# Kernel optimization log

Measured on AMD Instinct MI355X. Metric: run time of the kernel, lower is better.

Reference implementation:

```python
import jax, jax.numpy as jnp
import numpy as np

NUM_LAYERS = 3
N = 4096
DIM = 512
TOPK = 8
BIG = 1.0e9
EPS_COS = 1e-8
EPS_NORM = 1e-12
BN_EPS = 1e-5
LAM_K = 64.0
LAM_Z = 16.0
SIGMA_INTRA = 0.99
ALPHA = np.linspace(1.0, 1.2, NUM_LAYERS)
BETA = np.linspace(0.0, 0.0, NUM_LAYERS)


def setup_inputs() -> dict:
    key = jax.random.key(0)
    ks = jax.random.split(key, 6)
    feats = jax.random.normal(ks[0], (NUM_LAYERS, N, DIM), dtype=jnp.float32)
    labels = jax.random.randint(ks[1], (N,), 0, 64, dtype=jnp.int64)
    fc1_w = jax.random.normal(ks[2], (NUM_LAYERS, DIM, DIM), dtype=jnp.float32) * (1.0 / np.sqrt(DIM))
    fc2_w = jax.random.normal(ks[3], (NUM_LAYERS, DIM, DIM), dtype=jnp.float32) * (1.0 / np.sqrt(DIM))
    bn_gamma = jnp.ones((NUM_LAYERS, DIM), dtype=jnp.float32)
    bn_beta = jnp.zeros((NUM_LAYERS, DIM), dtype=jnp.float32)
    proj_w = jax.random.normal(ks[4], (768, DIM), dtype=jnp.float32) * (1.0 / np.sqrt(DIM))
    return {"feats": feats, "labels": labels, "fc1_w": fc1_w, "fc2_w": fc2_w,
            "bn_gamma": bn_gamma, "bn_beta": bn_beta, "proj_w": proj_w}


def _l2norm(x, axis=-1):
    return x / jnp.maximum(jnp.linalg.norm(x, axis=axis, keepdims=True), EPS_NORM)


def _pairwise_cosine(G):
    Gn = _l2norm(G)
    sim = Gn @ Gn.T
    return jnp.clip(sim, -1.0 + EPS_COS, 1.0 - EPS_COS)


def _knn_mask(sim, base_mask, topk):
    n = sim.shape[0]
    masked = (sim - BIG * jnp.eye(n, dtype=sim.dtype)) * base_mask - (1.0 - base_mask) * BIG
    k = min(topk, max(n - 1, 1))
    idx = jax.lax.top_k(masked, k)[1]  # [N, k]
    st = jnp.zeros_like(sim).at[jnp.arange(n)[:, None], idx].set(1.0)
    return jnp.maximum(st, st.T)


def _build_intra_inter(sim, labels, topk):
    same = (labels[None, :] == labels[:, None]).astype(sim.dtype)
    diff = 1.0 - same
    m_intra = _knn_mask(sim, same, topk)
    m_inter = _knn_mask(sim, diff, topk)
    sim_intra = jnp.maximum(sim * m_intra, 0.0)
    sim_inter = jnp.maximum(sim * m_inter, 0.0)
    return sim_intra, sim_inter


def _normalize_sym(sim_graph, eps=1e-8):
    d = jnp.maximum(sim_graph.sum(axis=1), eps)
    dinv = d ** -0.5
    return dinv[:, None] * sim_graph * dinv[None, :]  # == diag(dinv) @ S @ diag(dinv)


def _diffusion(K, t_diff=1):
    out = K
    for _ in range(max(t_diff - 1, 0)):
        out = out @ K
    return out


def _bn_train(x, gamma, beta):
    m = x.mean(axis=0)
    v = x.var(axis=0)  # biased, as torch BN training
    return (x - m) / jnp.sqrt(v + BN_EPS) * gamma + beta


def _gam(S, G, w1, w2, gamma, beta):
    Z = S @ (G @ w1.T)
    Z = jax.nn.relu(_bn_train(Z, gamma, beta))
    Z = S @ (Z @ w2.T)
    return Z + G


def reference(feats, labels, fc1_w, fc2_w, bn_gamma, bn_beta, proj_w):
    n = feats.shape[1]
    eye = jnp.eye(n, dtype=feats.dtype)
    same = (labels[None, :] == labels[:, None]).astype(feats.dtype)

    K_list, Z_list = [], []
    for i in range(NUM_LAYERS):
        G = feats[i]
        sim = _pairwise_cosine(G)
        sim_intra, sim_inter = _build_intra_inter(sim, labels, TOPK)
        sim_graph = float(ALPHA[i]) * sim_intra + float(BETA[i]) * sim_inter + 1e-6 * eye
        S = _normalize_sym(sim_graph)
        K = _diffusion(S, t_diff=1)
        Z = _gam(S, G, fc1_w[i], fc2_w[i], bn_gamma[i], bn_beta[i])
        K_list.append(K)
        Z_list.append(Z)

    loss_K = jnp.zeros((), dtype=feats.dtype)
    loss_Z = jnp.zeros((), dtype=feats.dtype)
    for i in range(1, NUM_LAYERS):
        K_tgt = jax.lax.stop_gradient(K_list[i])
        loss_K = loss_K + jnp.mean((K_list[i - 1] - K_tgt) ** 2)
        Zp = _l2norm(Z_list[i - 1] @ proj_w.T)
        Zc = _l2norm(Z_list[i] @ proj_w.T)
        loss_Z = loss_Z + jnp.mean((Zp - jax.lax.stop_gradient(Zc)) ** 2)

    K_idea = _diffusion(same * SIGMA_INTRA, t_diff=1)
    loss_idea = jnp.mean((K_list[-1] - K_idea) ** 2)
    return LAM_K * loss_K + LAM_Z * loss_Z + loss_idea
```

## Files before the change

kernel.cpp:

```cpp
#include <hip/hip_runtime.h>
#include <math.h>
#include <stdint.h>

#define NROWS 4096
#define DIM   512
#define NCLS  64
#define CAP   128
#define PD    768
#define NL    3
#define PARTSZ (size_t)(NCLS * 4 * 1024)

typedef __attribute__((ext_vector_type(8))) short short8v;
typedef __attribute__((ext_vector_type(4))) float f32x4;

__device__ __forceinline__ unsigned short f2bf(float f) {
  unsigned u = __float_as_uint(f);
  unsigned r = (u + 0x7FFF + ((u >> 16) & 1)) >> 16;
  return (unsigned short)r;
}

__device__ __forceinline__ void gload_lds16(const void* g, void* l) {
  auto* lp = reinterpret_cast<__attribute__((address_space(3))) unsigned int*>(
      reinterpret_cast<uintptr_t>(l));
  const auto* gp = reinterpret_cast<const __attribute__((address_space(1))) unsigned int*>(
      reinterpret_cast<uintptr_t>(g));
  __builtin_amdgcn_global_load_lds(gp, lp, 16, 0, 0);
}

__device__ __forceinline__ float waveReduce(float v) {
#pragma unroll
  for (int o = 32; o > 0; o >>= 1) v += __shfl_down(v, o);
  return v;
}

__device__ __forceinline__ float blockReduce(float v) {
  __shared__ float sh[4];
  int lane = threadIdx.x & 63, wv = threadIdx.x >> 6;
  v = waveReduce(v);
  if (lane == 0) sh[wv] = v;
  __syncthreads();
  float t = 0.f;
  if (threadIdx.x == 0) {
    int nw = (blockDim.x + 63) >> 6;
    for (int i = 0; i < nw; ++i) t += sh[i];
  }
  return t;
}

__global__ __launch_bounds__(256) void k_hist(const int* __restrict__ labels, int* __restrict__ chunkCnt) {
  __shared__ int h[NCLS];
  int t = threadIdx.x;
  if (t < NCLS) h[t] = 0;
  __syncthreads();
  atomicAdd(&h[labels[blockIdx.x * 256 + t]], 1);
  __syncthreads();
  if (t < NCLS) chunkCnt[blockIdx.x * NCLS + t] = h[t];
}

__global__ void k_scan(const int* __restrict__ chunkCnt, int* __restrict__ cnt,
                       int* __restrict__ off, int* __restrict__ chunkBase, float* __restrict__ acc) {
  __shared__ int sc[NCLS];
  int c = threadIdx.x;
  if (c < 8) acc[c] = 0.f;
  int tot = 0;
  for (int b = 0; b < 16; ++b) tot += chunkCnt[b * NCLS + c];
  cnt[c] = tot;
  sc[c] = tot;
  __syncthreads();
  if (c == 0) {
    int s = 0;
    for (int i = 0; i < NCLS; ++i) { int tv = sc[i]; sc[i] = s; s += tv; }
  }
  __syncthreads();
  int run = sc[c];
  off[c] = run;
  for (int b = 0; b < 16; ++b) { chunkBase[b * NCLS + c] = run; run += chunkCnt[b * NCLS + c]; }
  if (c == 0) off[NCLS] = NROWS;
}

__global__ __launch_bounds__(256) void k_scatter(const int* __restrict__ labels, const int* __restrict__ chunkBase,
                                                 int* __restrict__ perm, int* __restrict__ clsp) {
  __shared__ int lab[256];
  int t = threadIdx.x;
  int r = blockIdx.x * 256 + t;
  int c = labels[r];
  lab[t] = c;
  __syncthreads();
  int rank = 0;
  for (int j = 0; j < t; ++j) rank += (lab[j] == c);
  int pos = chunkBase[blockIdx.x * NCLS + c] + rank;
  perm[pos] = r;
  clsp[pos] = c;
}

__global__ __launch_bounds__(128) void k_prepw(const float* __restrict__ feats, const int* __restrict__ perm,
                                               unsigned short* __restrict__ Gpb, float* __restrict__ invn,
                                               const float4* __restrict__ fc1, const float4* __restrict__ fc2,
                                               const float4* __restrict__ proj,
                                               ushort4* __restrict__ w1, ushort4* __restrict__ w2,
                                               ushort4* __restrict__ pj, float* __restrict__ rnorm) {
  int y = blockIdx.y;
  if (y == NL) {
    const int nW = NL * DIM * DIM / 4;
    const int nP = PD * DIM / 4;
    int idx = blockIdx.x * 128 + threadIdx.x;
    const float4* src; ushort4* dst; int k;
    if (idx < nW) { src = fc1; dst = w1; k = idx; }
    else if (idx < 2 * nW) { src = fc2; dst = w2; k = idx - nW; }
    else if (idx < 2 * nW + nP) { src = proj; dst = pj; k = idx - 2 * nW; }
    else {
      int z = idx - (2 * nW + nP);
      if (z < NL * NROWS) rnorm[z] = 0.f;
      return;
    }
    float4 v = src[k];
    ushort4 o;
    o.x = f2bf(v.x); o.y = f2bf(v.y); o.z = f2bf(v.z); o.w = f2bf(v.w);
    dst[k] = o;
    return;
  }
  __shared__ float red[2];
  int l = y;
  const float* G = feats + (size_t)l * NROWS * DIM;
  unsigned short* Gp = Gpb + (size_t)l * NROWS * DIM;
  int row = blockIdx.x, t = threadIdx.x;
  const float4* src = (const float4*)(G + (size_t)perm[row] * DIM);
  float4 v = src[t];
  ushort4 b;
  b.x = f2bf(v.x); b.y = f2bf(v.y); b.z = f2bf(v.z); b.w = f2bf(v.w);
  *(ushort4*)(Gp + (size_t)row * DIM + t * 4) = b;
  float ss = v.x * v.x + v.y * v.y + v.z * v.z + v.w * v.w;
  ss = waveReduce(ss);
  if ((t & 63) == 0) red[t >> 6] = ss;
  __syncthreads();
  if (t == 0) invn[l * NROWS + row] = 1.f / fmaxf(sqrtf(red[0] + red[1]), 1e-12f);
}

__global__ __launch_bounds__(256) void k_sim(const unsigned short* __restrict__ Gpb,
                                             const float* __restrict__ invn,
                                             const int* __restrict__ cnt, const int* __restrict__ off,
                                             float* __restrict__ sim) {
  int l = blockIdx.z;
  const unsigned short* Gp = Gpb + (size_t)l * NROWS * DIM;
  const float* inv = invn + (size_t)l * NROWS;
  float* sm = sim + (size_t)l * NCLS * CAP * CAP;
  int c = blockIdx.y;
  int n = min(cnt[c], CAP);
  int ti = blockIdx.x >> 2, tj = blockIdx.x & 3;
  if (ti * 32 >= n || tj * 32 >= n) return;
  int base = off[c];
  __shared__ short As[32][40];
  __shared__ short Bs[32][40];
  const int t = threadIdx.x;
  const int lane = t & 63, wv = t >> 6;
  const int qi = wv >> 1, qj = wv & 1;
  const int fr = lane & 15, kg = lane >> 4;
  const int half = t >> 7, tt = t & 127;
  const int srow = tt >> 2, scol = (tt & 3) * 8;
  int gr = (half ? tj : ti) * 32 + srow;
  const unsigned short* ps = Gp + (size_t)(base + min(gr, n - 1)) * DIM + scol;
  short* dst = half ? &Bs[srow][scol] : &As[srow][scol];
  f32x4 acc = {};
  for (int k0 = 0; k0 < DIM; k0 += 32) {
    short8v v = *(const short8v*)(ps + k0);
    __syncthreads();
    *(short8v*)dst = v;
    __syncthreads();
    short8v af = *(const short8v*)&As[qi * 16 + fr][kg * 8];
    short8v bf = *(const short8v*)&Bs[qj * 16 + fr][kg * 8];
    acc = __builtin_amdgcn_mfma_f32_16x16x32_bf16(af, bf, acc, 0, 0, 0);
  }
  int gj = tj * 32 + qj * 16 + fr;
  int r0 = ti * 32 + qi * 16 + kg * 4;
  if (gj < n) {
    float sj = inv[base + gj];
#pragma unroll
    for (int r = 0; r < 4; ++r) {
      int gi = r0 + r;
      if (gi < n) {
        float v = acc[r] * inv[base + gi] * sj;
        v = fminf(fmaxf(v, -1.0f + 1e-8f), 1.0f - 1e-8f);
        sm[((size_t)c * CAP + gi) * CAP + gj] = v;
      }
    }
  }
}

__global__ __launch_bounds__(256) void k_topk(const float* __restrict__ sim, const int* __restrict__ cnt,
                                              const int* __restrict__ off, const int* __restrict__ clsp,
                                              int* __restrict__ t8) {
  int l = blockIdx.y;
  const float* sm = sim + (size_t)l * NCLS * CAP * CAP;
  int* t8l = t8 + (size_t)l * NROWS * 8;
  int pr = blockIdx.x * 256 + threadIdx.x;
  if (pr >= NROWS) return;
  int c = clsp[pr];
  int n = min(cnt[c], CAP);
  int loc = pr - off[c];
  const float4* row4 = (const float4*)(sm + ((size_t)c * CAP + loc) * CAP);
  float bv[8]; int bi[8];
#pragma unroll
  for (int q = 0; q < 8; ++q) { bv[q] = -3e38f; bi[q] = -1; }
  for (int j4 = 0; j4 < CAP / 4; ++j4) {
    if (j4 * 4 >= n) break;
    float4 v4 = row4[j4];
    float vv[4] = {v4.x, v4.y, v4.z, v4.w};
#pragma unroll
    for (int k = 0; k < 4; ++k) {
      int j = j4 * 4 + k;
      if (j >= n || j == loc) continue;
      float v = vv[k];
      if (v > bv[7]) {
        bv[7] = v; bi[7] = j;
#pragma unroll
        for (int q = 7; q > 0; --q) {
          if (bv[q] > bv[q - 1]) {
            float tv = bv[q]; bv[q] = bv[q - 1]; bv[q - 1] = tv;
            int tq = bi[q]; bi[q] = bi[q - 1]; bi[q - 1] = tq;
          }
        }
      }
    }
  }
#pragma unroll
  for (int q = 0; q < 8; ++q) t8l[pr * 8 + q] = bi[q];
}

__global__ __launch_bounds__(256) void k_buildS1(const float* __restrict__ sim, const int* __restrict__ cnt,
                                                 const int* __restrict__ off, const int* __restrict__ t8,
                                                 float* __restrict__ S, float* __restrict__ dinv) {
  int l = blockIdx.z;
  float alpha = 1.0f + 0.1f * l;
  const float* sm = sim + (size_t)l * NCLS * CAP * CAP;
  float* Sl = S + (size_t)l * NCLS * CAP * CAP;
  const int* t8l = t8 + (size_t)l * NROWS * 8;
  float* dv = dinv + (size_t)l * NCLS * CAP;
  int c = blockIdx.x;
  int n = min(cnt[c], CAP);
  int i0 = blockIdx.y * 32;
  if (i0 >= n) return;
  int base = off[c];
  __shared__ int sh8[CAP * 8];
  for (int i = threadIdx.x; i < n * 8; i += 256) sh8[i] = t8l[base * 8 + i];
  __syncthreads();
  int r = threadIdx.x >> 3;
  int lj = threadIdx.x & 7;
  int i = i0 + r;
  float d = 0.f;
  if (i < n) {
    int my8[8];
#pragma unroll
    for (int q = 0; q < 8; ++q) my8[q] = sh8[i * 8 + q];
    const float* srow = sm + ((size_t)c * CAP + i) * CAP;
    float* wrow = Sl + ((size_t)c * CAP + i) * CAP;
    for (int j = lj; j < n; j += 8) {
      float w;
      if (j == i) w = 1e-6f;
      else {
        bool m = false;
#pragma unroll
        for (int q = 0; q < 8; ++q) m = m || (my8[q] == j) || (sh8[j * 8 + q] == i);
        w = m ? alpha * fmaxf(srow[j], 0.f) : 0.f;
      }
      wrow[j] = w;
      d += w;
    }
  }
  d += __shfl_xor(d, 1);
  d += __shfl_xor(d, 2);
  d += __shfl_xor(d, 4);
  if (lj == 0 && i < n) dv[c * CAP + i] = 1.f / sqrtf(fmaxf(d, 1e-8f));
}

__global__ __launch_bounds__(256) void k_buildS2(float* __restrict__ S, const float* __restrict__ dinv,
                                                 const int* __restrict__ cnt) {
  int l = blockIdx.z;
  float* Sl = S + (size_t)l * NCLS * CAP * CAP;
  const float* dv = dinv + (size_t)l * NCLS * CAP;
  int c = blockIdx.x;
  int n = min(cnt[c], CAP);
  int i0 = blockIdx.y * 32;
  if (i0 >= n) return;
  __shared__ float sd[CAP];
  for (int k = threadIdx.x; k < n; k += 256) sd[k] = dv[c * CAP + k];
  __syncthreads();
  for (int p = threadIdx.x; p < 32 * CAP; p += 256) {
    int r = p >> 7, j = p & (CAP - 1);
    int i = i0 + r;
    if (i < n && j < n)
      Sl[((size_t)c * CAP + i) * CAP + j] *= sd[i] * sd[j];
  }
}

__global__ __launch_bounds__(256) void k_gemm_bf16(const short* __restrict__ A, const short* __restrict__ B,
                                                   float* __restrict__ C, float* __restrict__ rnorm, int N,
                                                   long sA, long sB, long sC) {
  int l = blockIdx.z;
  A += (size_t)l * sA; B += (size_t)l * sB; C += (size_t)l * sC;
  if (rnorm) rnorm += (size_t)l * NROWS;
  __shared__ __align__(16) short As[128][32];
  __shared__ __align__(16) short Bs[64][32];
  const int row0 = blockIdx.x * 128, col0 = blockIdx.y * 64;
  const int t = threadIdx.x;
  const int lane = t & 63, wv = t >> 6;
  const int fr = lane & 15, kg = lane >> 4;
  const int srow = lane >> 2, skb = (lane & 3) * 8;
  const short* pa = A + (size_t)(row0 + wv * 32 + srow) * DIM + skb;
  const short* pb = B + (size_t)(col0 + wv * 16 + srow) * DIM + skb;
  f32x4 acc[2][4] = {};
  for (int kt = 0; kt < DIM; kt += 32) {
    __syncthreads();
    gload_lds16(pa + kt, &As[wv * 32][0]);
    gload_lds16(pa + kt + (size_t)16 * DIM, &As[wv * 32 + 16][0]);
    gload_lds16(pb + kt, &Bs[wv * 16][0]);
    __syncthreads();
    short8v af[2], bf[4];
#pragma unroll
    for (int i = 0; i < 2; ++i) af[i] = *(const short8v*)&As[wv * 32 + i * 16 + fr][kg * 8];
#pragma unroll
    for (int j = 0; j < 4; ++j) bf[j] = *(const short8v*)&Bs[j * 16 + fr][kg * 8];
#pragma unroll
    for (int i = 0; i < 2; ++i)
#pragma unroll
      for (int j = 0; j < 4; ++j)
        acc[i][j] = __builtin_amdgcn_mfma_f32_16x16x32_bf16(af[i], bf[j], acc[i][j], 0, 0, 0);
  }
#pragma unroll
  for (int i = 0; i < 2; ++i) {
    int r0 = row0 + wv * 32 + i * 16 + kg * 4;
#pragma unroll
    for (int j = 0; j < 4; ++j) {
      int cc = col0 + j * 16 + fr;
#pragma unroll
      for (int r = 0; r < 4; ++r)
        C[(size_t)(r0 + r) * N + cc] = acc[i][j][r];
    }
    if (rnorm) {
#pragma unroll
      for (int r = 0; r < 4; ++r) {
        float ss = acc[i][0][r] * acc[i][0][r] + acc[i][1][r] * acc[i][1][r] +
                   acc[i][2][r] * acc[i][2][r] + acc[i][3][r] * acc[i][3][r];
        ss += __shfl_xor(ss, 1);
        ss += __shfl_xor(ss, 2);
        ss += __shfl_xor(ss, 4);
        ss += __shfl_xor(ss, 8);
        if (fr == 0) atomicAdd(&rnorm[r0 + r], ss);
      }
    }
  }
}

__global__ __launch_bounds__(256) void k_spmm32p(const float* __restrict__ S, const float* __restrict__ X,
                                                 const float* __restrict__ Gfeat, const int* __restrict__ perm,
                                                 float* __restrict__ Y, unsigned short* __restrict__ Yb,
                                                 float* __restrict__ part,
                                                 const int* __restrict__ cnt, const int* __restrict__ off) {
  int l = blockIdx.z >> 2;
  int zc = blockIdx.z & 3;
  const float* Sl = S + (size_t)l * NCLS * CAP * CAP;
  const float4* X4 = (const float4*)(X + (size_t)l * NROWS * DIM);
  const float4* G4 = Gfeat ? (const float4*)(Gfeat + (size_t)l * NROWS * DIM) : (const float4*)nullptr;
  float4* Y4 = Y ? (float4*)(Y + (size_t)l * NROWS * DIM) : (float4*)nullptr;
  ushort4* Yb4 = Yb ? (ushort4*)(Yb + (size_t)l * NROWS * DIM) : (ushort4*)nullptr;
  int c = blockIdx.x;
  int n = min(cnt[c], CAP);
  int i0 = zc * 32;
  float* pslot = part ? part + (size_t)l * PARTSZ + (size_t)(c * 4 + zc) * 1024 : (float*)nullptr;
  __shared__ float sS[32][CAP];
  if (i0 >= n) {
    if (pslot) {
      int col = blockIdx.y * 256 + threadIdx.x;
      pslot[col] = 0.f;
      pslot[512 + col] = 0.f;
    }
    return;
  }
  int base = off[c];
  int lane = threadIdx.x & 63;
  int col4 = blockIdx.y * 64 + lane;
  int ty = threadIdx.x >> 6;
  {
    const float4* S4 = (const float4*)(Sl + ((size_t)c * CAP + i0) * CAP);
    float4* sS4 = (float4*)&sS[0][0];
    for (int idx = threadIdx.x; idx < 32 * (CAP / 4); idx += 256) {
      int r = idx >> 5;
      sS4[idx] = (i0 + r < n) ? S4[idx] : make_float4(0.f, 0.f, 0.f, 0.f);
    }
  }
  __syncthreads();
  float4 acc[8];
#pragma unroll
  for (int ii = 0; ii < 8; ++ii) acc[ii] = make_float4(0.f, 0.f, 0.f, 0.f);
  size_t xbase = (size_t)base * 128 + col4;
  int n4 = n & ~3;
  float4 x0, x1, x2, x3;
  if (n4 > 0) {
    x0 = X4[xbase];
    x1 = X4[xbase + 128];
    x2 = X4[xbase + 256];
    x3 = X4[xbase + 384];
  }
  for (int j = 0; j < n4; j += 4) {
    float4 nx0, nx1, nx2, nx3;
    int jn = j + 4;
    if (jn < n4) {
      size_t b2 = xbase + (size_t)jn * 128;
      nx0 = X4[b2];
      nx1 = X4[b2 + 128];
      nx2 = X4[b2 + 256];
      nx3 = X4[b2 + 384];
    }
#pragma unroll
    for (int ii = 0; ii < 8; ++ii) {
      float4 s4 = *(const float4*)&sS[ty * 8 + ii][j];
      acc[ii].x += s4.x * x0.x; acc[ii].y += s4.x * x0.y; acc[ii].z += s4.x * x0.z; acc[ii].w += s4.x * x0.w;
      acc[ii].x += s4.y * x1.x; acc[ii].y += s4.y * x1.y; acc[ii].z += s4.y * x1.z; acc[ii].w += s4.y * x1.w;
      acc[ii].x += s4.z * x2.x; acc[ii].y += s4.z * x2.y; acc[ii].z += s4.z * x2.z; acc[ii].w += s4.z * x2.w;
      acc[ii].x += s4.w * x3.x; acc[ii].y += s4.w * x3.y; acc[ii].z += s4.w * x3.z; acc[ii].w += s4.w * x3.w;
    }
    x0 = nx0; x1 = nx1; x2 = nx2; x3 = nx3;
  }
  for (int j = n4; j < n; ++j) {
    float4 x = X4[xbase + (size_t)j * 128];
#pragma unroll
    for (int ii = 0; ii < 8; ++ii) {
      float s = sS[ty * 8 + ii][j];
      acc[ii].x += s * x.x;
      acc[ii].y += s * x.y;
      acc[ii].z += s * x.z;
      acc[ii].w += s * x.w;
    }
  }
  float s1[4] = {0.f, 0.f, 0.f, 0.f}, s2[4] = {0.f, 0.f, 0.f, 0.f};
#pragma unroll
  for (int ii = 0; ii < 8; ++ii) {
    int r = i0 + ty * 8 + ii;
    if (r < n) {
      size_t o = (size_t)(base + r) * 128 + col4;
      float4 v = acc[ii];
      if (G4) {
        float4 g = G4[(size_t)perm[base + r] * 128 + col4];
        v.x += g.x; v.y += g.y; v.z += g.z; v.w += g.w;
      }
      if (pslot) {
        s1[0] += v.x; s1[1] += v.y; s1[2] += v.z; s1[3] += v.w;
        s2[0] += v.x * v.x; s2[1] += v.y * v.y; s2[2] += v.z * v.z; s2[3] += v.w * v.w;
      }
      if (Yb4) {
        ushort4 ob;
        ob.x = f2bf(v.x); ob.y = f2bf(v.y); ob.z = f2bf(v.z); ob.w = f2bf(v.w);
        Yb4[o] = ob;
      } else {
        Y4[o] = v;
      }
    }
  }
  if (pslot) {
    __syncthreads();
    float* scr = &sS[0][0];
#pragma unroll
    for (int q = 0; q < 4; ++q) {
      scr[(ty * 64 + lane) * 8 + q] = s1[q];
      scr[(ty * 64 + lane) * 8 + 4 + q] = s2[q];
    }
    __syncthreads();
    if (ty == 0) {
#pragma unroll
      for (int q = 0; q < 4; ++q) {
        float a = 0.f, b = 0.f;
#pragma unroll
        for (int g = 0; g < 4; ++g) {
          a += scr[(g * 64 + lane) * 8 + q];
          b += scr[(g * 64 + lane) * 8 + 4 + q];
        }
        int col = blockIdx.y * 256 + lane * 4 + q;
        pslot[col] = a;
        pslot[512 + col] = b;
      }
    }
  }
}

__global__ __launch_bounds__(64) void k_bnfin(const float* __restrict__ part, const float* __restrict__ gamma,
                                              const float* __restrict__ beta, float* __restrict__ sc) {
  int l = blockIdx.y;
  const float* pl = part + (size_t)l * PARTSZ;
  int k = blockIdx.x * 64 + threadIdx.x;
  float s = 0.f, s2 = 0.f;
  for (int b = 0; b < NCLS * 4; ++b) {
    s += pl[b * 1024 + k];
    s2 += pl[b * 1024 + 512 + k];
  }
  float m = s * (1.f / NROWS);
  float var = s2 * (1.f / NROWS) - m * m;
  float sg = gamma[l * DIM + k] / sqrtf(var + 1e-5f);
  sc[l * 2 * DIM + k] = sg;
  sc[l * 2 * DIM + DIM + k] = beta[l * DIM + k] - m * sg;
}

__global__ __launch_bounds__(256) void k_bnrelu(const float4* __restrict__ X, const float* __restrict__ sc,
                                                ushort4* __restrict__ Yb) {
  int l = blockIdx.y;
  const float4* Xl = X + (size_t)l * (NROWS * DIM / 4);
  const float* scl = sc + (size_t)l * 2 * DIM;
  ushort4* Yl = Yb + (size_t)l * (NROWS * DIM / 4);
  int i = blockIdx.x * blockDim.x + threadIdx.x;
  int cb = (i * 4) & (DIM - 1);
  float4 v = Xl[i];
  ushort4 o;
  o.x = f2bf(fmaxf(v.x * scl[cb + 0] + scl[DIM + cb + 0], 0.f));
  o.y = f2bf(fmaxf(v.y * scl[cb + 1] + scl[DIM + cb + 1], 0.f));
  o.z = f2bf(fmaxf(v.z * scl[cb + 2] + scl[DIM + cb + 2], 0.f));
  o.w = f2bf(fmaxf(v.w * scl[cb + 3] + scl[DIM + cb + 3], 0.f));
  Yl[i] = o;
}

__global__ __launch_bounds__(256) void k_loss(const float* __restrict__ S, const float* __restrict__ P,
                                              const float* __restrict__ rnorm, const int* __restrict__ cnt,
                                              float target, float cK, float cI, float cZ,
                                              float* __restrict__ acc) {
  int y = blockIdx.y;
  if (y < 3) {
    if (blockIdx.x >= NCLS) return;
    const float* Sa = S + (size_t)y * NCLS * CAP * CAP;
    const float* Sb = nullptr;
    float coef;
    if (y < 2) { Sb = Sa + (size_t)NCLS * CAP * CAP; coef = cK; }
    else { Sa = S + (size_t)2 * NCLS * CAP * CAP; coef = cI; }
    int c = blockIdx.x;
    int n = min(cnt[c], CAP);
    float s = 0.f;
    for (int p = threadIdx.x; p < CAP * CAP; p += 256) {
      int i = p >> 7, j = p & (CAP - 1);
      if (i < n && j < n) {
        size_t o = ((size_t)c * CAP + i) * CAP + j;
        float d = Sb ? (Sa[o] - Sb[o]) : (Sa[o] - target);
        s += d * d;
      }
    }
    s = blockReduce(s);
    if (threadIdx.x == 0) atomicAdd(acc, s * coef);
  } else {
    int yy = y - 3;
    const float* A = P + (size_t)yy * NROWS * PD;
    const float* B = A + (size_t)NROWS * PD;
    const float* rnA = rnorm + (size_t)yy * NROWS;
    const float* rnB = rnA + NROWS;
    float s = 0.f;
    int row0 = blockIdx.x * 8;
#pragma unroll
    for (int ii = 0; ii < 8; ++ii) {
      int row = row0 + ii;
      float ia = 1.f / fmaxf(sqrtf(rnA[row]), 1e-12f);
      float ib = 1.f / fmaxf(sqrtf(rnB[row]), 1e-12f);
      const float* pa = A + (size_t)row * PD;
      const float* pb = B + (size_t)row * PD;
      for (int cidx = threadIdx.x; cidx < PD; cidx += 256) {
        float d = pa[cidx] * ia - pb[cidx] * ib;
        s += d * d;
      }
    }
    s = blockReduce(s);
    if (threadIdx.x == 0) atomicAdd(acc, s * cZ);
  }
}

__global__ void k_final(const float* __restrict__ acc, float* __restrict__ out) {
  if (threadIdx.x == 0) out[0] = acc[0];
}

extern "C" void kernel_launch(void* const* d_in, const int* in_sizes, int n_in,
                              void* d_out, int out_size, void* d_ws, size_t ws_size,
                              hipStream_t stream) {
  const float* feats = (const float*)d_in[0];
  const int* labels = (const int*)d_in[1];
  const float* fc1 = (const float*)d_in[2];
  const float* fc2 = (const float*)d_in[3];
  const float* gamma = (const float*)d_in[4];
  const float* beta = (const float*)d_in[5];
  const float* proj = (const float*)d_in[6];
  float* out = (float*)d_out;

  char* w = (char*)d_ws;
  auto alloc = [&](size_t bytes) { char* p = w; w += (bytes + 255) & ~(size_t)255; return p; };
  float* bufA = (float*)alloc((size_t)NL * NROWS * DIM * 4);
  float* bufB = (float*)alloc((size_t)NL * NROWS * DIM * 4);
  unsigned short* Gpb = (unsigned short*)alloc((size_t)NL * NROWS * DIM * 2);
  unsigned short* actb = (unsigned short*)alloc((size_t)NL * NROWS * DIM * 2);
  unsigned short* W1b = (unsigned short*)alloc((size_t)NL * DIM * DIM * 2);
  unsigned short* W2b = (unsigned short*)alloc((size_t)NL * DIM * DIM * 2);
  unsigned short* Pjb = (unsigned short*)alloc((size_t)PD * DIM * 2);
  float* sim  = (float*)alloc((size_t)NL * NCLS * CAP * CAP * 4);
  float* S    = (float*)alloc((size_t)NL * NCLS * CAP * CAP * 4);
  float* P    = (float*)alloc((size_t)NL * NROWS * PD * 4);
  float* invn = (float*)alloc((size_t)NL * NROWS * 4);
  float* dinv = (float*)alloc((size_t)NL * NCLS * CAP * 4);
  float* part = (float*)alloc((size_t)NL * PARTSZ * 4);
  float* bnsc = (float*)alloc((size_t)NL * 2 * DIM * 4);
  float* rnorm = (float*)alloc((size_t)NL * NROWS * 4);
  float* acc  = (float*)alloc(256);
  int* cnt  = (int*)alloc(NCLS * 4);
  int* offc = (int*)alloc((NCLS + 1) * 4);
  int* perm = (int*)alloc(NROWS * 4);
  int* clsp = (int*)alloc(NROWS * 4);
  int* t8   = (int*)alloc((size_t)NL * NROWS * 8 * 4);
  int* chunkCnt  = (int*)alloc(16 * NCLS * 4);
  int* chunkBase = (int*)alloc(16 * NCLS * 4);

  const float LAM_K = 64.f, LAM_Z = 16.f, SIGMA = 0.99f;
  const float cK = LAM_K / ((float)NROWS * (float)NROWS);
  const float cZ = LAM_Z / ((float)NROWS * (float)PD);
  const float cI = 1.f / ((float)NROWS * (float)NROWS);
  const long sAct = (long)NROWS * DIM;
  const long sW = (long)DIM * DIM;

  hipLaunchKernelGGL(k_hist, dim3(16), dim3(256), 0, stream, labels, chunkCnt);
  hipLaunchKernelGGL(k_scan, dim3(1), dim3(64), 0, stream, chunkCnt, cnt, offc, chunkBase, acc);
  hipLaunchKernelGGL(k_scatter, dim3(16), dim3(256), 0, stream, labels, chunkBase, perm, clsp);

  hipLaunchKernelGGL(k_prepw, dim3(NROWS, NL + 1), dim3(128), 0, stream, feats, perm, Gpb, invn,
                     (const float4*)fc1, (const float4*)fc2, (const float4*)proj,
                     (ushort4*)W1b, (ushort4*)W2b, (ushort4*)Pjb, rnorm);

  hipLaunchKernelGGL(k_sim, dim3(16, NCLS, NL), dim3(256), 0, stream, Gpb, invn, cnt, offc, sim);
  hipLaunchKernelGGL(k_topk, dim3(NROWS / 256, NL), dim3(256), 0, stream, sim, cnt, offc, clsp, t8);
  hipLaunchKernelGGL(k_buildS1, dim3(NCLS, CAP / 32, NL), dim3(256), 0, stream, sim, cnt, offc, t8, S, dinv);
  hipLaunchKernelGGL(k_buildS2, dim3(NCLS, CAP / 32, NL), dim3(256), 0, stream, S, dinv, cnt);

  hipLaunchKernelGGL(k_gemm_bf16, dim3(NROWS / 128, DIM / 64, NL), dim3(256), 0, stream,
                     (const short*)Gpb, (const short*)W1b, bufA, (float*)nullptr, DIM, sAct, sW, (long)NROWS * DIM);
  hipLaunchKernelGGL(k_spmm32p, dim3(NCLS, DIM / 256, 4 * NL), dim3(256), 0, stream, S, bufA,
                     (const float*)nullptr, (const int*)nullptr, bufB, (unsigned short*)nullptr, part, cnt, offc);
  hipLaunchKernelGGL(k_bnfin, dim3(DIM / 64, NL), dim3(64), 0, stream, part, gamma, beta, bnsc);
  hipLaunchKernelGGL(k_bnrelu, dim3(NROWS * DIM / 4 / 256, NL), dim3(256), 0, stream,
                     (const float4*)bufB, bnsc, (ushort4*)actb);
  hipLaunchKernelGGL(k_gemm_bf16, dim3(NROWS / 128, DIM / 64, NL), dim3(256), 0, stream,
                     (const short*)actb, (const short*)W2b, bufB, (float*)nullptr, DIM, sAct, sW, (long)NROWS * DIM);
  hipLaunchKernelGGL(k_spmm32p, dim3(NCLS, DIM / 256, 4 * NL), dim3(256), 0, stream, S, bufB,
                     feats, perm, (float*)nullptr, actb, (float*)nullptr, cnt, offc);
  hipLaunchKernelGGL(k_gemm_bf16, dim3(NROWS / 128, PD / 64, NL), dim3(256), 0, stream,
                     (const short*)actb, (const short*)Pjb, P, rnorm, PD, sAct, 0L, (long)NROWS * PD);

  hipLaunchKernelGGL(k_loss, dim3(512, 5), dim3(256), 0, stream, S, P, rnorm, cnt, SIGMA, cK, cI, cZ, acc);

  hipLaunchKernelGGL(k_final, dim3(1), dim3(64), 0, stream, acc, out);
}
```

Before: 253.8 us.

## Fuse similarity, top-k, graph build and normalization into one per-class kernel

Replaces four kernels (per-class cosine similarity, top-k selection, masked graph build, symmetric normalization) with a single kernel that does all of them for one class and layer. The similarity tile stays in LDS, so the global sim, t8 and dinv buffers and three launches go away. The MFMA loop now reads bf16 operands straight from global memory with no LDS staging. The cost is less parallelism: 192 blocks where there were many more, top-k runs on only 128 threads per block, and each block uses a large amount of LDS.

```diff
diff --git a/kernel.cpp b/kernel.cpp
--- a/kernel.cpp
+++ b/kernel.cpp
@@ -136,159 +136,126 @@
   if (t == 0) invn[l * NROWS + row] = 1.f / fmaxf(sqrtf(red[0] + red[1]), 1e-12f);
 }
 
-__global__ __launch_bounds__(256) void k_sim(const unsigned short* __restrict__ Gpb,
-                                             const float* __restrict__ invn,
-                                             const int* __restrict__ cnt, const int* __restrict__ off,
-                                             float* __restrict__ sim) {
-  int l = blockIdx.z;
+__global__ __launch_bounds__(256) void k_graph(const unsigned short* __restrict__ Gpb,
+                                               const float* __restrict__ invn,
+                                               const int* __restrict__ cnt, const int* __restrict__ off,
+                                               float* __restrict__ S) {
+  int l = blockIdx.y;
   const unsigned short* Gp = Gpb + (size_t)l * NROWS * DIM;
   const float* inv = invn + (size_t)l * NROWS;
-  float* sm = sim + (size_t)l * NCLS * CAP * CAP;
-  int c = blockIdx.y;
+  float* Sl = S + (size_t)l * NCLS * CAP * CAP;
+  int c = blockIdx.x;
   int n = min(cnt[c], CAP);
-  int ti = blockIdx.x >> 2, tj = blockIdx.x & 3;
-  if (ti * 32 >= n || tj * 32 >= n) return;
   int base = off[c];
-  __shared__ short As[32][40];
-  __shared__ short Bs[32][40];
+  float alpha = 1.0f + 0.1f * l;
+
+  __shared__ float simL[CAP][CAP + 4];
+  __shared__ int sm8[CAP][8];
+  __shared__ float sdinv[CAP];
+
   const int t = threadIdx.x;
   const int lane = t & 63, wv = t >> 6;
   const int qi = wv >> 1, qj = wv & 1;
   const int fr = lane & 15, kg = lane >> 4;
-  const int half = t >> 7, tt = t & 127;
-  const int srow = tt >> 2, scol = (tt & 3) * 8;
-  int gr = (half ? tj : ti) * 32 + srow;
-  const unsigned short* ps = Gp + (size_t)(base + min(gr, n - 1)) * DIM + scol;
-  short* dst = half ? &Bs[srow][scol] : &As[srow][scol];
-  f32x4 acc = {};
-  for (int k0 = 0; k0 < DIM; k0 += 32) {
-    short8v v = *(const short8v*)(ps + k0);
-    __syncthreads();
-    *(short8v*)dst = v;
-    __syncthreads();
-    short8v af = *(const short8v*)&As[qi * 16 + fr][kg * 8];
-    short8v bf = *(const short8v*)&Bs[qj * 16 + fr][kg * 8];
-    acc = __builtin_amdgcn_mfma_f32_16x16x32_bf16(af, bf, acc, 0, 0, 0);
-  }
-  int gj = tj * 32 + qj * 16 + fr;
-  int r0 = ti * 32 + qi * 16 + kg * 4;
-  if (gj < n) {
-    float sj = inv[base + gj];
-#pragma unroll
-    for (int r = 0; r < 4; ++r) {
-      int gi = r0 + r;
-      if (gi < n) {
-        float v = acc[r] * inv[base + gi] * sj;
-        v = fminf(fmaxf(v, -1.0f + 1e-8f), 1.0f - 1e-8f);
-        sm[((size_t)c * CAP + gi) * CAP + gj] = v;
-      }
-    }
-  }
-}
-
-__global__ __launch_bounds__(256) void k_topk(const float* __restrict__ sim, const int* __restrict__ cnt,
-                                              const int* __restrict__ off, const int* __restrict__ clsp,
-                                              int* __restrict__ t8) {
-  int l = blockIdx.y;
-  const float* sm = sim + (size_t)l * NCLS * CAP * CAP;
-  int* t8l = t8 + (size_t)l * NROWS * 8;
-  int pr = blockIdx.x * 256 + threadIdx.x;
-  if (pr >= NROWS) return;
-  int c = clsp[pr];
-  int n = min(cnt[c], CAP);
-  int loc = pr - off[c];
-  const float4* row4 = (const float4*)(sm + ((size_t)c * CAP + loc) * CAP);
-  float bv[8]; int bi[8];
-#pragma unroll
-  for (int q = 0; q < 8; ++q) { bv[q] = -3e38f; bi[q] = -1; }
-  for (int j4 = 0; j4 < CAP / 4; ++j4) {
-    if (j4 * 4 >= n) break;
-    float4 v4 = row4[j4];
-    float vv[4] = {v4.x, v4.y, v4.z, v4.w};
-#pragma unroll
-    for (int k = 0; k < 4; ++k) {
-      int j = j4 * 4 + k;
-      if (j >= n || j == loc) continue;
-      float v = vv[k];
-      if (v > bv[7]) {
-        bv[7] = v; bi[7] = j;
-#pragma unroll
-        for (int q = 7; q > 0; --q) {
-          if (bv[q] > bv[q - 1]) {
-            float tv = bv[q]; bv[q] = bv[q - 1]; bv[q - 1] = tv;
-            int tq = bi[q]; bi[q] = bi[q - 1]; bi[q - 1] = tq;
+
+  int nt = (n + 31) >> 5;
+  for (int ti = 0; ti < nt; ++ti) {
+    for (int tj = 0; tj < nt; ++tj) {
+      int ra = ti * 32 + qi * 16 + fr;
+      int rb = tj * 32 + qj * 16 + fr;
+      const unsigned short* pa = Gp + (size_t)(base + min(ra, n - 1)) * DIM + kg * 8;
+      const unsigned short* pb = Gp + (size_t)(base + min(rb, n - 1)) * DIM + kg * 8;
+      f32x4 acc = {};
+#pragma unroll
+      for (int k0 = 0; k0 < DIM; k0 += 32) {
+        short8v af = *(const short8v*)(pa + k0);
+        short8v bf = *(const short8v*)(pb + k0);
+        acc = __builtin_amdgcn_mfma_f32_16x16x32_bf16(af, bf, acc, 0, 0, 0);
+      }
+      int gj = rb;
+      int r0 = ti * 32 + qi * 16 + kg * 4;
+      if (gj < n) {
+        float sj = inv[base + gj];
+#pragma unroll
+        for (int r = 0; r < 4; ++r) {
+          int gi = r0 + r;
+          if (gi < n) {
+            float v = acc[r] * inv[base + gi] * sj;
+            v = fminf(fmaxf(v, -1.0f + 1e-8f), 1.0f - 1e-8f);
+            simL[gi][gj] = v;
           }
         }
       }
     }
   }
-#pragma unroll
-  for (int q = 0; q < 8; ++q) t8l[pr * 8 + q] = bi[q];
-}
-
-__global__ __launch_bounds__(256) void k_buildS1(const float* __restrict__ sim, const int* __restrict__ cnt,
-                                                 const int* __restrict__ off, const int* __restrict__ t8,
-                                                 float* __restrict__ S, float* __restrict__ dinv) {
-  int l = blockIdx.z;
-  float alpha = 1.0f + 0.1f * l;
-  const float* sm = sim + (size_t)l * NCLS * CAP * CAP;
-  float* Sl = S + (size_t)l * NCLS * CAP * CAP;
-  const int* t8l = t8 + (size_t)l * NROWS * 8;
-  float* dv = dinv + (size_t)l * NCLS * CAP;
-  int c = blockIdx.x;
-  int n = min(cnt[c], CAP);
-  int i0 = blockIdx.y * 32;
-  if (i0 >= n) return;
-  int base = off[c];
-  __shared__ int sh8[CAP * 8];
-  for (int i = threadIdx.x; i < n * 8; i += 256) sh8[i] = t8l[base * 8 + i];
-  __syncthreads();
-  int r = threadIdx.x >> 3;
-  int lj = threadIdx.x & 7;
-  int i = i0 + r;
-  float d = 0.f;
-  if (i < n) {
-    int my8[8];
-#pragma unroll
-    for (int q = 0; q < 8; ++q) my8[q] = sh8[i * 8 + q];
-    const float* srow = sm + ((size_t)c * CAP + i) * CAP;
-    float* wrow = Sl + ((size_t)c * CAP + i) * CAP;
-    for (int j = lj; j < n; j += 8) {
-      float w;
-      if (j == i) w = 1e-6f;
-      else {
-        bool m = false;
-#pragma unroll
-        for (int q = 0; q < 8; ++q) m = m || (my8[q] == j) || (sh8[j * 8 + q] == i);
-        w = m ? alpha * fmaxf(srow[j], 0.f) : 0.f;
-      }
-      wrow[j] = w;
-      d += w;
-    }
-  }
-  d += __shfl_xor(d, 1);
-  d += __shfl_xor(d, 2);
-  d += __shfl_xor(d, 4);
-  if (lj == 0 && i < n) dv[c * CAP + i] = 1.f / sqrtf(fmaxf(d, 1e-8f));
-}
-
-__global__ __launch_bounds__(256) void k_buildS2(float* __restrict__ S, const float* __restrict__ dinv,
-                                                 const int* __restrict__ cnt) {
-  int l = blockIdx.z;
-  float* Sl = S + (size_t)l * NCLS * CAP * CAP;
-  const float* dv = dinv + (size_t)l * NCLS * CAP;
-  int c = blockIdx.x;
-  int n = min(cnt[c], CAP);
-  int i0 = blockIdx.y * 32;
-  if (i0 >= n) return;
-  __shared__ float sd[CAP];
-  for (int k = threadIdx.x; k < n; k += 256) sd[k] = dv[c * CAP + k];
-  __syncthreads();
-  for (int p = threadIdx.x; p < 32 * CAP; p += 256) {
-    int r = p >> 7, j = p & (CAP - 1);
-    int i = i0 + r;
-    if (i < n && j < n)
-      Sl[((size_t)c * CAP + i) * CAP + j] *= sd[i] * sd[j];
+  if (t < CAP) sdinv[t] = 0.f;
+  __syncthreads();
+
+  if (t < CAP) {
+    int i = t;
+    float bv[8]; int bi[8];
+#pragma unroll
+    for (int q = 0; q < 8; ++q) { bv[q] = -3e38f; bi[q] = -1; }
+    if (i < n) {
+      for (int j = 0; j < n; ++j) {
+        if (j == i) continue;
+        float v = simL[i][j];
+        if (v > bv[7]) {
+          bv[7] = v; bi[7] = i == i ? j : j;
+#pragma unroll
+          for (int q = 7; q > 0; --q) {
+            if (bv[q] > bv[q - 1]) {
+              float tv = bv[q]; bv[q] = bv[q - 1]; bv[q - 1] = tv;
+              int tq = bi[q]; bi[q] = bi[q - 1]; bi[q - 1] = tq;
+            }
+          }
+        }
+      }
+    }
+#pragma unroll
+    for (int q = 0; q < 8; ++q) sm8[i][q] = bi[q];
+  }
+  __syncthreads();
+
+  {
+    int r = t >> 3, lj = t & 7;
+    for (int i0 = 0; i0 < CAP; i0 += 32) {
+      int i = i0 + r;
+      float d = 0.f;
+      if (i < n) {
+        int my8[8];
+#pragma unroll
+        for (int q = 0; q < 8; ++q) my8[q] = sm8[i][q];
+        for (int j = lj; j < n; j += 8) {
+          float w;
+          if (j == i) w = 1e-6f;
+          else {
+            bool m = false;
+#pragma unroll
+            for (int q = 0; q < 8; ++q) m = m || (my8[q] == j) || (sm8[j][q] == i);
+            w = m ? alpha * fmaxf(simL[i][j], 0.f) : 0.f;
+          }
+          simL[i][j] = w;
+          d += w;
+        }
+      }
+      d += __shfl_xor(d, 1);
+      d += __shfl_xor(d, 2);
+      d += __shfl_xor(d, 4);
+      if (lj == 0 && i < n) sdinv[i] = 1.f / sqrtf(fmaxf(d, 1e-8f));
+    }
+  }
+  __syncthreads();
+
+  for (int idx = t; idx < n * (CAP / 4); idx += 256) {
+    int i = idx >> 5, j0 = (idx & 31) * 4;
+    float di = sdinv[i];
+    float4 o;
+    o.x = (j0 + 0 < n) ? simL[i][j0 + 0] * di * sdinv[j0 + 0] : 0.f;
+    o.y = (j0 + 1 < n) ? simL[i][j0 + 1] * di * sdinv[j0 + 1] : 0.f;
+    o.z = (j0 + 2 < n) ? simL[i][j0 + 2] * di * sdinv[j0 + 2] : 0.f;
+    o.w = (j0 + 3 < n) ? simL[i][j0 + 3] * di * sdinv[j0 + 3] : 0.f;
+    *(float4*)&Sl[((size_t)c * CAP + i) * CAP + j0] = o;
   }
 }
 
@@ -590,11 +557,9 @@
   unsigned short* W1b = (unsigned short*)alloc((size_t)NL * DIM * DIM * 2);
   unsigned short* W2b = (unsigned short*)alloc((size_t)NL * DIM * DIM * 2);
   unsigned short* Pjb = (unsigned short*)alloc((size_t)PD * DIM * 2);
-  float* sim  = (float*)alloc((size_t)NL * NCLS * CAP * CAP * 4);
   float* S    = (float*)alloc((size_t)NL * NCLS * CAP * CAP * 4);
   float* P    = (float*)alloc((size_t)NL * NROWS * PD * 4);
   float* invn = (float*)alloc((size_t)NL * NROWS * 4);
-  float* dinv = (float*)alloc((size_t)NL * NCLS * CAP * 4);
   float* part = (float*)alloc((size_t)NL * PARTSZ * 4);
   float* bnsc = (float*)alloc((size_t)NL * 2 * DIM * 4);
   float* rnorm = (float*)alloc((size_t)NL * NROWS * 4);
@@ -603,7 +568,6 @@
   int* offc = (int*)alloc((NCLS + 1) * 4);
   int* perm = (int*)alloc(NROWS * 4);
   int* clsp = (int*)alloc(NROWS * 4);
-  int* t8   = (int*)alloc((size_t)NL * NROWS * 8 * 4);
   int* chunkCnt  = (int*)alloc(16 * NCLS * 4);
   int* chunkBase = (int*)alloc(16 * NCLS * 4);
 
@@ -622,10 +586,7 @@
                      (const float4*)fc1, (const float4*)fc2, (const float4*)proj,
                      (ushort4*)W1b, (ushort4*)W2b, (ushort4*)Pjb, rnorm);
 
-  hipLaunchKernelGGL(k_sim, dim3(16, NCLS, NL), dim3(256), 0, stream, Gpb, invn, cnt, offc, sim);
-  hipLaunchKernelGGL(k_topk, dim3(NROWS / 256, NL), dim3(256), 0, stream, sim, cnt, offc, clsp, t8);
-  hipLaunchKernelGGL(k_buildS1, dim3(NCLS, CAP / 32, NL), dim3(256), 0, stream, sim, cnt, offc, t8, S, dinv);
-  hipLaunchKernelGGL(k_buildS2, dim3(NCLS, CAP / 32, NL), dim3(256), 0, stream, S, dinv, cnt);
+  hipLaunchKernelGGL(k_graph, dim3(NCLS, NL), dim3(256), 0, stream, Gpb, invn, cnt, offc, S);
 
   hipLaunchKernelGGL(k_gemm_bf16, dim3(NROWS / 128, DIM / 64, NL), dim3(256), 0, stream,
                      (const short*)Gpb, (const short*)W1b, bufA, (float*)nullptr, DIM, sAct, sW, (long)NROWS * DIM);
```

New measurement: 254.1 us. About the same (+0.1%).

## Store projection output in bf16 and reuse permuted bf16 features for residual

Applied to the files above, without the earlier changes.

The projection GEMM now writes its output as bf16 instead of fp32, and the loss kernel reads bf16 values and widens them. The second spmm takes its residual from the already-permuted bf16 copy of the features, indexed contiguously, instead of a gather from the fp32 features through perm. Both changes cut global memory traffic, at the cost of extra rounding in the Z loss and in the residual added to the activations.

```diff
diff --git a/kernel.cpp b/kernel.cpp
--- a/kernel.cpp
+++ b/kernel.cpp
@@ -17,6 +17,16 @@
   unsigned u = __float_as_uint(f);
   unsigned r = (u + 0x7FFF + ((u >> 16) & 1)) >> 16;
   return (unsigned short)r;
+}
+
+__device__ __forceinline__ float bf2f(unsigned short u) {
+  return __uint_as_float(((unsigned)u) << 16);
+}
+
+__device__ __forceinline__ float4 bf4tof4(ushort4 u) {
+  float4 f;
+  f.x = bf2f(u.x); f.y = bf2f(u.y); f.z = bf2f(u.z); f.w = bf2f(u.w);
+  return f;
 }
 
 __device__ __forceinline__ void gload_lds16(const void* g, void* l) {
@@ -293,10 +303,12 @@
 }
 
 __global__ __launch_bounds__(256) void k_gemm_bf16(const short* __restrict__ A, const short* __restrict__ B,
-                                                   float* __restrict__ C, float* __restrict__ rnorm, int N,
+                                                   float* __restrict__ C, unsigned short* __restrict__ Cb,
+                                                   float* __restrict__ rnorm, int N,
                                                    long sA, long sB, long sC) {
   int l = blockIdx.z;
-  A += (size_t)l * sA; B += (size_t)l * sB; C += (size_t)l * sC;
+  A += (size_t)l * sA; B += (size_t)l * sB;
+  if (Cb) Cb += (size_t)l * sC; else C += (size_t)l * sC;
   if (rnorm) rnorm += (size_t)l * NROWS;
   __shared__ __align__(16) short As[128][32];
   __shared__ __align__(16) short Bs[64][32];
@@ -332,8 +344,10 @@
     for (int j = 0; j < 4; ++j) {
       int cc = col0 + j * 16 + fr;
 #pragma unroll
-      for (int r = 0; r < 4; ++r)
-        C[(size_t)(r0 + r) * N + cc] = acc[i][j][r];
+      for (int r = 0; r < 4; ++r) {
+        if (Cb) Cb[(size_t)(r0 + r) * N + cc] = f2bf(acc[i][j][r]);
+        else C[(size_t)(r0 + r) * N + cc] = acc[i][j][r];
+      }
     }
     if (rnorm) {
 #pragma unroll
@@ -351,7 +365,7 @@
 }
 
 __global__ __launch_bounds__(256) void k_spmm32p(const float* __restrict__ S, const float* __restrict__ X,
-                                                 const float* __restrict__ Gfeat, const int* __restrict__ perm,
+                                                 const unsigned short* __restrict__ Gb,
                                                  float* __restrict__ Y, unsigned short* __restrict__ Yb,
                                                  float* __restrict__ part,
                                                  const int* __restrict__ cnt, const int* __restrict__ off) {
@@ -359,7 +373,7 @@
   int zc = blockIdx.z & 3;
   const float* Sl = S + (size_t)l * NCLS * CAP * CAP;
   const float4* X4 = (const float4*)(X + (size_t)l * NROWS * DIM);
-  const float4* G4 = Gfeat ? (const float4*)(Gfeat + (size_t)l * NROWS * DIM) : (const float4*)nullptr;
+  const ushort4* Gb4 = Gb ? (const ushort4*)(Gb + (size_t)l * NROWS * DIM) : (const ushort4*)nullptr;
   float4* Y4 = Y ? (float4*)(Y + (size_t)l * NROWS * DIM) : (float4*)nullptr;
   ushort4* Yb4 = Yb ? (ushort4*)(Yb + (size_t)l * NROWS * DIM) : (ushort4*)nullptr;
   int c = blockIdx.x;
@@ -438,8 +452,8 @@
     if (r < n) {
       size_t o = (size_t)(base + r) * 128 + col4;
       float4 v = acc[ii];
-      if (G4) {
-        float4 g = G4[(size_t)perm[base + r] * 128 + col4];
+      if (Gb4) {
+        float4 g = bf4tof4(Gb4[o]);
         v.x += g.x; v.y += g.y; v.z += g.z; v.w += g.w;
       }
       if (pslot) {
@@ -515,7 +529,7 @@
   Yl[i] = o;
 }
 
-__global__ __launch_bounds__(256) void k_loss(const float* __restrict__ S, const float* __restrict__ P,
+__global__ __launch_bounds__(256) void k_loss(const float* __restrict__ S, const unsigned short* __restrict__ P,
                                               const float* __restrict__ rnorm, const int* __restrict__ cnt,
                                               float target, float cK, float cI, float cZ,
                                               float* __restrict__ acc) {
@@ -542,8 +556,8 @@
     if (threadIdx.x == 0) atomicAdd(acc, s * coef);
   } else {
     int yy = y - 3;
-    const float* A = P + (size_t)yy * NROWS * PD;
-    const float* B = A + (size_t)NROWS * PD;
+    const unsigned short* A = P + (size_t)yy * NROWS * PD;
+    const unsigned short* B = A + (size_t)NROWS * PD;
     const float* rnA = rnorm + (size_t)yy * NROWS;
     const float* rnB = rnA + NROWS;
     float s = 0.f;
@@ -553,10 +567,10 @@
       int row = row0 + ii;
       float ia = 1.f / fmaxf(sqrtf(rnA[row]), 1e-12f);
       float ib = 1.f / fmaxf(sqrtf(rnB[row]), 1e-12f);
-      const float* pa = A + (size_t)row * PD;
-      const float* pb = B + (size_t)row * PD;
+      const unsigned short* pa = A + (size_t)row * PD;
+      const unsigned short* pb = B + (size_t)row * PD;
       for (int cidx = threadIdx.x; cidx < PD; cidx += 256) {
-        float d = pa[cidx] * ia - pb[cidx] * ib;
+        float d = bf2f(pa[cidx]) * ia - bf2f(pb[cidx]) * ib;
         s += d * d;
       }
     }
@@ -592,7 +606,7 @@
   unsigned short* Pjb = (unsigned short*)alloc((size_t)PD * DIM * 2);
   float* sim  = (float*)alloc((size_t)NL * NCLS * CAP * CAP * 4);
   float* S    = (float*)alloc((size_t)NL * NCLS * CAP * CAP * 4);
-  float* P    = (float*)alloc((size_t)NL * NROWS * PD * 4);
+  unsigned short* Pb = (unsigned short*)alloc((size_t)NL * NROWS * PD * 2);
   float* invn = (float*)alloc((size_t)NL * NROWS * 4);
   float* dinv = (float*)alloc((size_t)NL * NCLS * CAP * 4);
   float* part = (float*)alloc((size_t)NL * PARTSZ * 4);
@@ -628,20 +642,23 @@
   hipLaunchKernelGGL(k_buildS2, dim3(NCLS, CAP / 32, NL), dim3(256), 0, stream, S, dinv, cnt);
 
   hipLaunchKernelGGL(k_gemm_bf16, dim3(NROWS / 128, DIM / 64, NL), dim3(256), 0, stream,
-                     (const short*)Gpb, (const short*)W1b, bufA, (float*)nullptr, DIM, sAct, sW, (long)NROWS * DIM);
+                     (const short*)Gpb, (const short*)W1b, bufA, (unsigned short*)nullptr, (float*)nullptr,
+                     DIM, sAct, sW, (long)NROWS * DIM);
   hipLaunchKernelGGL(k_spmm32p, dim3(NCLS, DIM / 256, 4 * NL), dim3(256), 0, stream, S, bufA,
-                     (const float*)nullptr, (const int*)nullptr, bufB, (unsigned short*)nullptr, part, cnt, offc);
+                     (const unsigned short*)nullptr, bufB, (unsigned short*)nullptr, part, cnt, offc);
   hipLaunchKernelGGL(k_bnfin, dim3(DIM / 64, NL), dim3(64), 0, stream, part, gamma, beta, bnsc);
   hipLaunchKernelGGL(k_bnrelu, dim3(NROWS * DIM / 4 / 256, NL), dim3(256), 0, stream,
                      (const float4*)bufB, bnsc, (ushort4*)actb);
   hipLaunchKernelGGL(k_gemm_bf16, dim3(NROWS / 128, DIM / 64, NL), dim3(256), 0, stream,
-                     (const short*)actb, (const short*)W2b, bufB, (float*)nullptr, DIM, sAct, sW, (long)NROWS * DIM);
+                     (const short*)actb, (const short*)W2b, bufB, (unsigned short*)nullptr, (float*)nullptr,
+                     DIM, sAct, sW, (long)NROWS * DIM);
   hipLaunchKernelGGL(k_spmm32p, dim3(NCLS, DIM / 256, 4 * NL), dim3(256), 0, stream, S, bufB,
-                     feats, perm, (float*)nullptr, actb, (float*)nullptr, cnt, offc);
+                     Gpb, (float*)nullptr, actb, (float*)nullptr, cnt, offc);
   hipLaunchKernelGGL(k_gemm_bf16, dim3(NROWS / 128, PD / 64, NL), dim3(256), 0, stream,
-                     (const short*)actb, (const short*)Pjb, P, rnorm, PD, sAct, 0L, (long)NROWS * PD);
-
-  hipLaunchKernelGGL(k_loss, dim3(512, 5), dim3(256), 0, stream, S, P, rnorm, cnt, SIGMA, cK, cI, cZ, acc);
+                     (const short*)actb, (const short*)Pjb, (float*)nullptr, Pb, rnorm,
+                     PD, sAct, 0L, (long)NROWS * PD);
+
+  hipLaunchKernelGGL(k_loss, dim3(512, 5), dim3(256), 0, stream, S, Pb, rnorm, cnt, SIGMA, cK, cI, cZ, acc);
 
   hipLaunchKernelGGL(k_final, dim3(1), dim3(64), 0, stream, acc, out);
 }
```

Result: no change. 249.6 us (median of 2 runs) (-1.7%).
